# Optimization experiments

Measured on AMD Instinct MI355X. Metric: run time of the kernel, lower is better.

## Reference

```python
import jax, jax.numpy as jnp
import numpy as np

DIM = 1024
HEADS = 8
SCALE = 64 ** (-0.5)  # module uses dimHead=64 even though per-head c = DIM//HEADS = 128
LN_EPS = 1e-3  # keras LayerNormalization default


def _layernorm(t, g, b):
    mu = jnp.mean(t, axis=-1, keepdims=True)
    var = jnp.mean(jnp.square(t - mu), axis=-1, keepdims=True)
    return (t - mu) * jax.lax.rsqrt(var + LN_EPS) * g + b


def setup_inputs() -> dict:
    key = jax.random.key(0)
    ks = jax.random.split(key, 4)
    B, N, D = 4, 2048, DIM
    x = jax.random.normal(ks[0], (B, N, D), dtype=jnp.float32)
    w3 = jax.random.normal(ks[1], (D, 3 * D), dtype=jnp.float32) * (1.0 / np.sqrt(D))
    w1 = jax.random.normal(ks[2], (D, 4 * D), dtype=jnp.float32) * (1.0 / np.sqrt(D))
    w2 = jax.random.normal(ks[3], (4 * D, D), dtype=jnp.float32) * (1.0 / np.sqrt(4 * D))
    return {
        "x": x,
        "ln_g": jnp.ones((D,), jnp.float32),
        "ln_b": jnp.zeros((D,), jnp.float32),
        "w3": w3,
        "b3": jnp.zeros((3 * D,), jnp.float32),
        "w1": w1,
        "b1": jnp.zeros((4 * D,), jnp.float32),
        "w2": w2,
        "b2": jnp.zeros((D,), jnp.float32),
    }


def reference(x, ln_g, ln_b, w3, b3, w1, b1, w2, b2):
    B, N, D = x.shape
    H = HEADS
    C = D // H  # per-head channel dim

    # --- attention branch ---
    y = _layernorm(x, ln_g, ln_b)
    qkv = jax.nn.relu(y @ w3 + b3)  # [B, N, 3D] (note: relu on QKV, as in source)
    # einops 'b n (c h i) -> i b h n c' with i=3: last axis factors as (C, H, 3)
    qkv = qkv.reshape(B, N, C, H, 3)
    qkv = jnp.transpose(qkv, (4, 0, 3, 1, 2))  # [3, B, H, N, C]
    q, k, v = qkv[0], qkv[1], qkv[2]
    scores = jnp.einsum("bhqc,bhkc->bhqk", q, k) * SCALE
    attn = jax.nn.softmax(scores, axis=-1)
    o = jnp.einsum("bhqk,bhkc->bhqc", attn, v)  # [B, H, N, C]
    # 'b h n c -> b n (h c)'
    o = jnp.transpose(o, (0, 2, 1, 3)).reshape(B, N, H * C)
    y = o + x

    # --- MLP branch (shared layernorm params; dropout is identity at inference) ---
    y1 = _layernorm(y, ln_g, ln_b)
    mlp = jax.nn.relu(y1 @ w1 + b1) @ w2 + b2
    return mlp + y
```

## Files before the change

kernel.cpp:

```cpp
#include <hip/hip_runtime.h>
#include <hip/hip_bf16.h>
#include <cstdint>

typedef __attribute__((ext_vector_type(8))) __bf16 bf16x8;
typedef __attribute__((ext_vector_type(4))) float f32x4;
typedef unsigned short u16;

#define DEV static __device__ __forceinline__

constexpr float ATT_SCALE = 0.125f;
constexpr float LN_EPS = 1e-3f;

DEV void gload16(const void* g, void* l) {
  __builtin_amdgcn_global_load_lds((__attribute__((address_space(1))) void*)(g),
                                   (__attribute__((address_space(3))) void*)(l),
                                   16, 0, 0);
}

DEV u16 f2b(float f) { __hip_bfloat16 h = __float2bfloat16(f); return __builtin_bit_cast(u16, h); }

template<int PERM>
__global__ __launch_bounds__(256)
void k_transpose(const float* __restrict__ in, __hip_bfloat16* __restrict__ out,
                 int R, int C) {
  __shared__ float t[64][65];
  int d0 = blockIdx.x * 64, k0 = blockIdx.y * 64;
  int tid = threadIdx.x;
  int c64 = tid & 63, r4 = tid >> 6;
#pragma unroll
  for (int i = 0; i < 16; i++) {
    int kr = i * 4 + r4;
    t[c64][kr] = in[(size_t)(k0 + kr) * C + d0 + c64];
  }
  __syncthreads();
#pragma unroll
  for (int i = 0; i < 16; i++) {
    int dr = i * 4 + r4;
    int d = d0 + dr;
    int jp = PERM ? ((d % 3) * 1024 + ((d / 3) & 7) * 128 + (d / 24)) : d;
    out[(size_t)jp * R + k0 + c64] = __float2bfloat16(t[dr][c64]);
  }
}

__global__ __launch_bounds__(256)
void k_ln(const float* __restrict__ in, const float* __restrict__ g,
          const float* __restrict__ b, __hip_bfloat16* __restrict__ out) {
  int row = blockIdx.x, tid = threadIdx.x;
  const float4* in4 = (const float4*)(in + (size_t)row * 1024);
  float4 v = in4[tid];
  float s = v.x + v.y + v.z + v.w;
  float ss = v.x * v.x + v.y * v.y + v.z * v.z + v.w * v.w;
#pragma unroll
  for (int off = 32; off; off >>= 1) { s += __shfl_down(s, off); ss += __shfl_down(ss, off); }
  __shared__ float red[8];
  int w = tid >> 6, lane = tid & 63;
  if (lane == 0) { red[w] = s; red[4 + w] = ss; }
  __syncthreads();
  if (tid == 0) {
    float S = red[0] + red[1] + red[2] + red[3];
    float SS = red[4] + red[5] + red[6] + red[7];
    float mu = S * (1.f / 1024.f);
    float var = SS * (1.f / 1024.f) - mu * mu;
    red[0] = mu; red[1] = rsqrtf(var + LN_EPS);
  }
  __syncthreads();
  float mu = red[0], rs = red[1];
  int c = tid * 4;
  ushort4 o;
  o.x = f2b((v.x - mu) * rs * g[c + 0] + b[c + 0]);
  o.y = f2b((v.y - mu) * rs * g[c + 1] + b[c + 1]);
  o.z = f2b((v.z - mu) * rs * g[c + 2] + b[c + 2]);
  o.w = f2b((v.w - mu) * rs * g[c + 3] + b[c + 3]);
  ((ushort4*)((u16*)out + (size_t)row * 1024))[tid] = o;
}

template<int MODE>
__global__ __launch_bounds__(256, 2)
void k_gemm(const __hip_bfloat16* __restrict__ A,
            const __hip_bfloat16* __restrict__ Bt,
            const float* __restrict__ bias,
            const float* __restrict__ resid,
            float* __restrict__ outF,
            __hip_bfloat16* __restrict__ outQ,
            __hip_bfloat16* __restrict__ outK,
            __hip_bfloat16* __restrict__ outV,
            int K, int Nout) {
  __shared__ alignas(16) __hip_bfloat16 Asm[128 * 32];
  __shared__ alignas(16) __hip_bfloat16 Bsm[128 * 32];
  int tid = threadIdx.x, w = tid >> 6, lane = tid & 63;
  int wr = w >> 1, wc = w & 1;
  int lr = lane >> 4, lc = lane & 15;
  int m0 = blockIdx.y * 128, n0 = blockIdx.x * 128;
  f32x4 acc[4][4] = {};
  const __hip_bfloat16* aG = A + (size_t)(m0 + (tid >> 2)) * K + (tid & 3) * 8;
  const __hip_bfloat16* bG = Bt + (size_t)(n0 + (tid >> 2)) * K + (tid & 3) * 8;
  char* aB = (char*)Asm + w * 1024;
  char* bB = (char*)Bsm + w * 1024;
  for (int k0 = 0; k0 < K; k0 += 32) {
    gload16(aG + k0, aB);
    gload16(aG + (size_t)64 * K + k0, aB + 4096);
    gload16(bG + k0, bB);
    gload16(bG + (size_t)64 * K + k0, bB + 4096);
    __syncthreads();
    bf16x8 af[4], bfr[4];
#pragma unroll
    for (int mi = 0; mi < 4; mi++)
      af[mi] = *(const bf16x8*)(Asm + (wr * 64 + mi * 16 + lc) * 32 + lr * 8);
#pragma unroll
    for (int ni = 0; ni < 4; ni++)
      bfr[ni] = *(const bf16x8*)(Bsm + (wc * 64 + ni * 16 + lc) * 32 + lr * 8);
#pragma unroll
    for (int mi = 0; mi < 4; mi++)
#pragma unroll
      for (int ni = 0; ni < 4; ni++)
        acc[mi][ni] = __builtin_amdgcn_mfma_f32_16x16x32_bf16(af[mi], bfr[ni], acc[mi][ni], 0, 0, 0);
    __syncthreads();
  }
#pragma unroll
  for (int mi = 0; mi < 4; mi++) {
#pragma unroll
    for (int ni = 0; ni < 4; ni++) {
      int jp = n0 + wc * 64 + ni * 16 + lc;
#pragma unroll
      for (int r = 0; r < 4; r++) {
        int m = m0 + wr * 64 + mi * 16 + lr * 4 + r;
        float v = acc[mi][ni][r];
        if (MODE == 0) {
          int i = jp >> 10, h = (jp >> 7) & 7, c = jp & 127;
          v += bias[c * 24 + h * 3 + i];
          v = fmaxf(v, 0.f);
          __hip_bfloat16 bv = __float2bfloat16(v);
          int b_ = m >> 11, n = m & 2047;
          size_t bh = (size_t)(b_ * 8 + h);
          if (i == 0)      outQ[(bh * 2048 + n) * 128 + c] = bv;
          else if (i == 1) outK[(bh * 2048 + n) * 128 + c] = bv;
          else             outV[(bh * 128 + c) * 2048 + n] = bv;
        } else if (MODE == 1) {
          v += bias[jp];
          v = fmaxf(v, 0.f);
          outQ[(size_t)m * Nout + jp] = __float2bfloat16(v);
        } else {
          v += bias[jp] + resid[(size_t)m * Nout + jp];
          outF[(size_t)m * Nout + jp] = v;
        }
      }
    }
  }
}

__global__ __launch_bounds__(256, 1)
void k_attn(const __hip_bfloat16* __restrict__ qb,
            const __hip_bfloat16* __restrict__ kb,
            const __hip_bfloat16* __restrict__ vtb,
            const float* __restrict__ x,
            float* __restrict__ y) {
  __shared__ alignas(16) __hip_bfloat16 Kl[64 * 128];
  __shared__ alignas(16) __hip_bfloat16 Vl[128 * 64];
  __shared__ alignas(16) __hip_bfloat16 Pl[4 * 32 * 72];
  int tid = threadIdx.x, w = tid >> 6, lane = tid & 63;
  int lr = lane >> 4, lc = lane & 15;
  int qt = blockIdx.x, bh = blockIdx.y;
  int b_ = bh >> 3, h = bh & 7;
  int q0 = qt * 128;
  size_t bhN = (size_t)bh * 2048;

  bf16x8 qf[2][4];
#pragma unroll
  for (int mi = 0; mi < 2; mi++)
#pragma unroll
    for (int ks = 0; ks < 4; ks++)
      qf[mi][ks] = *(const bf16x8*)(qb + (bhN + q0 + w * 32 + mi * 16 + lc) * 128 + ks * 32 + lr * 8);

  f32x4 oacc[2][8] = {};
  float mrun[2][4], lrun[2][4];
#pragma unroll
  for (int mi = 0; mi < 2; mi++)
#pragma unroll
    for (int r = 0; r < 4; r++) { mrun[mi][r] = -1e30f; lrun[mi][r] = 0.f; }

  const __hip_bfloat16* kG = kb + (bhN + (tid >> 4)) * 128 + (tid & 15) * 8;
  const __hip_bfloat16* vG = vtb + ((size_t)bh * 128 + (tid >> 3)) * 2048 + (tid & 7) * 8;
  char* kB = (char*)Kl + w * 1024;
  char* vB = (char*)Vl + w * 1024;

  for (int kv0 = 0; kv0 < 2048; kv0 += 64) {
#pragma unroll
    for (int p = 0; p < 4; p++)
      gload16(kG + (size_t)(kv0 + p * 16) * 128, kB + p * 4096);
#pragma unroll
    for (int p = 0; p < 4; p++)
      gload16(vG + kv0 + (size_t)p * 32 * 2048, vB + p * 4096);
    __syncthreads();

    f32x4 sf[2][4] = {};
#pragma unroll
    for (int ks = 0; ks < 4; ks++) {
      bf16x8 kfr[4];
#pragma unroll
      for (int ni = 0; ni < 4; ni++)
        kfr[ni] = *(const bf16x8*)(Kl + (ni * 16 + lc) * 128 + ks * 32 + lr * 8);
#pragma unroll
      for (int mi = 0; mi < 2; mi++)
#pragma unroll
        for (int ni = 0; ni < 4; ni++)
          sf[mi][ni] = __builtin_amdgcn_mfma_f32_16x16x32_bf16(qf[mi][ks], kfr[ni], sf[mi][ni], 0, 0, 0);
    }

#pragma unroll
    for (int mi = 0; mi < 2; mi++) {
#pragma unroll
      for (int r = 0; r < 4; r++) {
        float tmax = fmaxf(fmaxf(sf[mi][0][r], sf[mi][1][r]), fmaxf(sf[mi][2][r], sf[mi][3][r]));
#pragma unroll
        for (int off = 1; off < 16; off <<= 1) tmax = fmaxf(tmax, __shfl_xor(tmax, off, 16));
        tmax *= ATT_SCALE;
        float mnew = fmaxf(mrun[mi][r], tmax);
        float alpha = __expf(mrun[mi][r] - mnew);
        mrun[mi][r] = mnew;
        float rs = 0.f;
#pragma unroll
        for (int ni = 0; ni < 4; ni++) {
          float p = __expf(sf[mi][ni][r] * ATT_SCALE - mnew);
          sf[mi][ni][r] = p;
          rs += p;
        }
#pragma unroll
        for (int off = 1; off < 16; off <<= 1) rs += __shfl_xor(rs, off, 16);
        lrun[mi][r] = lrun[mi][r] * alpha + rs;
#pragma unroll
        for (int nc = 0; nc < 8; nc++) oacc[mi][nc][r] *= alpha;
      }
    }

#pragma unroll
    for (int mi = 0; mi < 2; mi++)
#pragma unroll
      for (int ni = 0; ni < 4; ni++)
#pragma unroll
        for (int r = 0; r < 4; r++)
          Pl[w * 2304 + (mi * 16 + lr * 4 + r) * 72 + ni * 16 + lc] = __float2bfloat16(sf[mi][ni][r]);
    asm volatile("s_waitcnt lgkmcnt(0)" ::: "memory");

#pragma unroll
    for (int ks2 = 0; ks2 < 2; ks2++) {
      bf16x8 pa[2];
#pragma unroll
      for (int mi = 0; mi < 2; mi++)
        pa[mi] = *(const bf16x8*)(Pl + w * 2304 + (mi * 16 + lc) * 72 + ks2 * 32 + lr * 8);
#pragma unroll
      for (int nc = 0; nc < 8; nc++) {
        bf16x8 vf = *(const bf16x8*)(Vl + (nc * 16 + lc) * 64 + ks2 * 32 + lr * 8);
#pragma unroll
        for (int mi = 0; mi < 2; mi++)
          oacc[mi][nc] = __builtin_amdgcn_mfma_f32_16x16x32_bf16(pa[mi], vf, oacc[mi][nc], 0, 0, 0);
      }
    }
    __syncthreads();
  }

#pragma unroll
  for (int mi = 0; mi < 2; mi++)
#pragma unroll
    for (int r = 0; r < 4; r++) {
      int n = q0 + w * 32 + mi * 16 + lr * 4 + r;
      float inv = 1.f / lrun[mi][r];
      size_t base = ((size_t)(b_ * 2048 + n)) * 1024 + h * 128;
#pragma unroll
      for (int nc = 0; nc < 8; nc++) {
        int c = nc * 16 + lc;
        y[base + c] = oacc[mi][nc][r] * inv + x[base + c];
      }
    }
}

extern "C" void kernel_launch(void* const* d_in, const int* in_sizes, int n_in,
                              void* d_out, int out_size, void* d_ws, size_t ws_size,
                              hipStream_t stream) {
  const float* x   = (const float*)d_in[0];
  const float* lng = (const float*)d_in[1];
  const float* lnb = (const float*)d_in[2];
  const float* w3  = (const float*)d_in[3];
  const float* b3  = (const float*)d_in[4];
  const float* w1  = (const float*)d_in[5];
  const float* b1  = (const float*)d_in[6];
  const float* w2  = (const float*)d_in[7];
  const float* b2  = (const float*)d_in[8];
  float* out = (float*)d_out;

  constexpr size_t M = 8192;
  __hip_bfloat16* w3t  = (__hip_bfloat16*)d_ws;
  __hip_bfloat16* w1t  = w3t + (size_t)3072 * 1024;
  __hip_bfloat16* w2t  = w1t + (size_t)4096 * 1024;
  __hip_bfloat16* xln  = w2t + (size_t)4096 * 1024;
  __hip_bfloat16* qb   = xln + M * 1024;
  __hip_bfloat16* kbuf = qb + M * 1024;
  __hip_bfloat16* vtb  = kbuf + M * 1024;
  __hip_bfloat16* hmid = qb;

  k_transpose<1><<<dim3(48, 16), 256, 0, stream>>>(w3, w3t, 1024, 3072);
  k_transpose<0><<<dim3(64, 16), 256, 0, stream>>>(w1, w1t, 1024, 4096);
  k_transpose<0><<<dim3(16, 64), 256, 0, stream>>>(w2, w2t, 4096, 1024);
  k_ln<<<dim3(M), 256, 0, stream>>>(x, lng, lnb, xln);
  k_gemm<0><<<dim3(24, 64), 256, 0, stream>>>(xln, w3t, b3, nullptr, nullptr,
                                              qb, kbuf, vtb, 1024, 3072);
  k_attn<<<dim3(16, 32), 256, 0, stream>>>(qb, kbuf, vtb, x, out);
  k_ln<<<dim3(M), 256, 0, stream>>>(out, lng, lnb, xln);
  k_gemm<1><<<dim3(32, 64), 256, 0, stream>>>(xln, w1t, b1, nullptr, nullptr,
                                              hmid, nullptr, nullptr, 1024, 4096);
  k_gemm<2><<<dim3(8, 64), 256, 0, stream>>>(hmid, w2t, b2, out, out,
                                             nullptr, nullptr, nullptr, 4096, 1024);
}
```

Before: 611.4 us.

## Halve attention query tile, raise occupancy, and XOR-swizzle K/V LDS layout

```diff
diff --git a/kernel.cpp b/kernel.cpp
--- a/kernel.cpp
+++ b/kernel.cpp
@@ -148,7 +148,7 @@
   }
 }
 
-__global__ __launch_bounds__(256, 1)
+__global__ __launch_bounds__(256, 3)
 void k_attn(const __hip_bfloat16* __restrict__ qb,
             const __hip_bfloat16* __restrict__ kb,
             const __hip_bfloat16* __restrict__ vtb,
@@ -156,30 +156,31 @@
             float* __restrict__ y) {
   __shared__ alignas(16) __hip_bfloat16 Kl[64 * 128];
   __shared__ alignas(16) __hip_bfloat16 Vl[128 * 64];
-  __shared__ alignas(16) __hip_bfloat16 Pl[4 * 32 * 72];
+  __shared__ alignas(16) __hip_bfloat16 Pl[4 * 16 * 72];
   int tid = threadIdx.x, w = tid >> 6, lane = tid & 63;
   int lr = lane >> 4, lc = lane & 15;
+  int sxz = (lc & 7) << 3;
   int qt = blockIdx.x, bh = blockIdx.y;
   int b_ = bh >> 3, h = bh & 7;
-  int q0 = qt * 128;
+  int q0 = qt * 64;
   size_t bhN = (size_t)bh * 2048;
 
-  bf16x8 qf[2][4];
-#pragma unroll
-  for (int mi = 0; mi < 2; mi++)
-#pragma unroll
-    for (int ks = 0; ks < 4; ks++)
-      qf[mi][ks] = *(const bf16x8*)(qb + (bhN + q0 + w * 32 + mi * 16 + lc) * 128 + ks * 32 + lr * 8);
-
-  f32x4 oacc[2][8] = {};
-  float mrun[2][4], lrun[2][4];
-#pragma unroll
-  for (int mi = 0; mi < 2; mi++)
-#pragma unroll
-    for (int r = 0; r < 4; r++) { mrun[mi][r] = -1e30f; lrun[mi][r] = 0.f; }
-
-  const __hip_bfloat16* kG = kb + (bhN + (tid >> 4)) * 128 + (tid & 15) * 8;
-  const __hip_bfloat16* vG = vtb + ((size_t)bh * 128 + (tid >> 3)) * 2048 + (tid & 7) * 8;
+  bf16x8 qf[4];
+#pragma unroll
+  for (int ks = 0; ks < 4; ks++)
+    qf[ks] = *(const bf16x8*)(qb + (bhN + q0 + w * 16 + lc) * 128 + ks * 32 + lr * 8);
+
+  f32x4 oacc[8] = {};
+  float mrun[4], lrun[4];
+#pragma unroll
+  for (int r = 0; r < 4; r++) { mrun[r] = -1e30f; lrun[r] = 0.f; }
+
+  int krow = tid >> 4;
+  int kcol = ((tid & 15) * 8) ^ ((krow & 7) << 3);
+  const __hip_bfloat16* kG = kb + (bhN + krow) * 128 + kcol;
+  int vrow = tid >> 3;
+  int vcol = ((tid & 7) * 8) ^ ((vrow & 7) << 3);
+  const __hip_bfloat16* vG = vtb + ((size_t)bh * 128 + vrow) * 2048 + vcol;
   char* kB = (char*)Kl + w * 1024;
   char* vB = (char*)Vl + w * 1024;
 
@@ -192,85 +193,71 @@
       gload16(vG + kv0 + (size_t)p * 32 * 2048, vB + p * 4096);
     __syncthreads();
 
-    f32x4 sf[2][4] = {};
+    f32x4 sf[4] = {};
 #pragma unroll
     for (int ks = 0; ks < 4; ks++) {
       bf16x8 kfr[4];
 #pragma unroll
       for (int ni = 0; ni < 4; ni++)
-        kfr[ni] = *(const bf16x8*)(Kl + (ni * 16 + lc) * 128 + ks * 32 + lr * 8);
-#pragma unroll
-      for (int mi = 0; mi < 2; mi++)
-#pragma unroll
-        for (int ni = 0; ni < 4; ni++)
-          sf[mi][ni] = __builtin_amdgcn_mfma_f32_16x16x32_bf16(qf[mi][ks], kfr[ni], sf[mi][ni], 0, 0, 0);
-    }
-
-#pragma unroll
-    for (int mi = 0; mi < 2; mi++) {
-#pragma unroll
-      for (int r = 0; r < 4; r++) {
-        float tmax = fmaxf(fmaxf(sf[mi][0][r], sf[mi][1][r]), fmaxf(sf[mi][2][r], sf[mi][3][r]));
-#pragma unroll
-        for (int off = 1; off < 16; off <<= 1) tmax = fmaxf(tmax, __shfl_xor(tmax, off, 16));
-        tmax *= ATT_SCALE;
-        float mnew = fmaxf(mrun[mi][r], tmax);
-        float alpha = __expf(mrun[mi][r] - mnew);
-        mrun[mi][r] = mnew;
-        float rs = 0.f;
-#pragma unroll
-        for (int ni = 0; ni < 4; ni++) {
-          float p = __expf(sf[mi][ni][r] * ATT_SCALE - mnew);
-          sf[mi][ni][r] = p;
-          rs += p;
-        }
-#pragma unroll
-        for (int off = 1; off < 16; off <<= 1) rs += __shfl_xor(rs, off, 16);
-        lrun[mi][r] = lrun[mi][r] * alpha + rs;
-#pragma unroll
-        for (int nc = 0; nc < 8; nc++) oacc[mi][nc][r] *= alpha;
+        kfr[ni] = *(const bf16x8*)(Kl + (ni * 16 + lc) * 128 + ((ks * 32 + lr * 8) ^ sxz));
+#pragma unroll
+      for (int ni = 0; ni < 4; ni++)
+        sf[ni] = __builtin_amdgcn_mfma_f32_16x16x32_bf16(qf[ks], kfr[ni], sf[ni], 0, 0, 0);
+    }
+
+#pragma unroll
+    for (int r = 0; r < 4; r++) {
+      float tmax = fmaxf(fmaxf(sf[0][r], sf[1][r]), fmaxf(sf[2][r], sf[3][r]));
+#pragma unroll
+      for (int off = 1; off < 16; off <<= 1) tmax = fmaxf(tmax, __shfl_xor(tmax, off, 16));
+      tmax *= ATT_SCALE;
+      float mnew = fmaxf(mrun[r], tmax);
+      float alpha = __expf(mrun[r] - mnew);
+      mrun[r] = mnew;
+      float rs = 0.f;
+#pragma unroll
+      for (int ni = 0; ni < 4; ni++) {
+        float p = __expf(sf[ni][r] * ATT_SCALE - mnew);
+        sf[ni][r] = p;
+        rs += p;
       }
-    }
-
-#pragma unroll
-    for (int mi = 0; mi < 2; mi++)
-#pragma unroll
-      for (int ni = 0; ni < 4; ni++)
-#pragma unroll
-        for (int r = 0; r < 4; r++)
-          Pl[w * 2304 + (mi * 16 + lr * 4 + r) * 72 + ni * 16 + lc] = __float2bfloat16(sf[mi][ni][r]);
+#pragma unroll
+      for (int off = 1; off < 16; off <<= 1) rs += __shfl_xor(rs, off, 16);
+      lrun[r] = lrun[r] * alpha + rs;
+#pragma unroll
+      for (int nc = 0; nc < 8; nc++) oacc[nc][r] *= alpha;
+    }
+
+#pragma unroll
+    for (int ni = 0; ni < 4; ni++)
+#pragma unroll
+      for (int r = 0; r < 4; r++)
+        Pl[w * 1152 + (lr * 4 + r) * 72 + ni * 16 + lc] = __float2bfloat16(sf[ni][r]);
     asm volatile("s_waitcnt lgkmcnt(0)" ::: "memory");
 
 #pragma unroll
     for (int ks2 = 0; ks2 < 2; ks2++) {
-      bf16x8 pa[2];
-#pragma unroll
-      for (int mi = 0; mi < 2; mi++)
-        pa[mi] = *(const bf16x8*)(Pl + w * 2304 + (mi * 16 + lc) * 72 + ks2 * 32 + lr * 8);
+      bf16x8 pa = *(const bf16x8*)(Pl + w * 1152 + lc * 72 + ks2 * 32 + lr * 8);
 #pragma unroll
       for (int nc = 0; nc < 8; nc++) {
-        bf16x8 vf = *(const bf16x8*)(Vl + (nc * 16 + lc) * 64 + ks2 * 32 + lr * 8);
-#pragma unroll
-        for (int mi = 0; mi < 2; mi++)
-          oacc[mi][nc] = __builtin_amdgcn_mfma_f32_16x16x32_bf16(pa[mi], vf, oacc[mi][nc], 0, 0, 0);
+        bf16x8 vf = *(const bf16x8*)(Vl + (nc * 16 + lc) * 64 + ((ks2 * 32 + lr * 8) ^ sxz));
+        oacc[nc] = __builtin_amdgcn_mfma_f32_16x16x32_bf16(pa, vf, oacc[nc], 0, 0, 0);
       }
     }
     __syncthreads();
   }
 
 #pragma unroll
-  for (int mi = 0; mi < 2; mi++)
-#pragma unroll
-    for (int r = 0; r < 4; r++) {
-      int n = q0 + w * 32 + mi * 16 + lr * 4 + r;
-      float inv = 1.f / lrun[mi][r];
-      size_t base = ((size_t)(b_ * 2048 + n)) * 1024 + h * 128;
-#pragma unroll
-      for (int nc = 0; nc < 8; nc++) {
-        int c = nc * 16 + lc;
-        y[base + c] = oacc[mi][nc][r] * inv + x[base + c];
-      }
-    }
+  for (int r = 0; r < 4; r++) {
+    int n = q0 + w * 16 + lr * 4 + r;
+    float inv = 1.f / lrun[r];
+    size_t base = ((size_t)(b_ * 2048 + n)) * 1024 + h * 128;
+#pragma unroll
+    for (int nc = 0; nc < 8; nc++) {
+      int c = nc * 16 + lc;
+      y[base + c] = oacc[nc][r] * inv + x[base + c];
+    }
+  }
 }
 
 extern "C" void kernel_launch(void* const* d_in, const int* in_sizes, int n_in,
@@ -303,7 +290,7 @@
   k_ln<<<dim3(M), 256, 0, stream>>>(x, lng, lnb, xln);
   k_gemm<0><<<dim3(24, 64), 256, 0, stream>>>(xln, w3t, b3, nullptr, nullptr,
                                               qb, kbuf, vtb, 1024, 3072);
-  k_attn<<<dim3(16, 32), 256, 0, stream>>>(qb, kbuf, vtb, x, out);
+  k_attn<<<dim3(32, 32), 256, 0, stream>>>(qb, kbuf, vtb, x, out);
   k_ln<<<dim3(M), 256, 0, stream>>>(out, lng, lnb, xln);
   k_gemm<1><<<dim3(32, 64), 256, 0, stream>>>(xln, w1t, b1, nullptr, nullptr,
                                               hmid, nullptr, nullptr, 1024, 4096);
```

Result: faster. 569.4 us (-6.9%).
